# Kernel tuning notes

Measured on AMD Instinct MI355X. Metric: run time of the kernel, lower is better.

The kernel has to match this reference:

```python
import jax, jax.numpy as jnp
import numpy as np

T, B, I, H = 512, 64, 512, 1024

def setup_inputs() -> dict:
    key = jax.random.key(0)
    k1, k2, k3 = jax.random.split(key, 3)
    scale = 1.0 / np.sqrt(I + H)  # torch Linear default-ish scale
    return {
        "inputs": jax.random.normal(k1, (T, B, I), dtype=jnp.float32),
        "W": jax.random.normal(k2, (4 * H, I + H), dtype=jnp.float32) * scale,
        "b": jax.random.normal(k3, (4 * H,), dtype=jnp.float32) * scale,
    }

def reference(inputs, W, b):
    Bsz = inputs.shape[1]
    Hd = W.shape[0] // 4
    hx0 = jnp.zeros((Bsz, Hd), dtype=inputs.dtype)
    cx0 = jnp.zeros((Bsz, Hd), dtype=inputs.dtype)
    Wt = W.T  # [I+H, 4H]

    def step(carry, x):
        hx, cx = carry
        combined = jnp.concatenate([x, hx], axis=1)       # [B, I+H]
        gates = combined @ Wt + b                          # [B, 4H]
        f, i, g, o = jnp.split(gates, 4, axis=1)
        f = jax.nn.sigmoid(f)
        i = jax.nn.sigmoid(i)
        g = jnp.tanh(g)
        o = jax.nn.sigmoid(o)
        cx = f * cx + i * g
        hx = o * jnp.tanh(cx)
        return (hx, cx), hx

    (hx, cx), stacked = jax.lax.scan(step, (hx0, cx0), inputs)
    return stacked, (hx, cx)
```

## Files before the change

### kernel.cpp

```cpp
#include <hip/hip_runtime.h>
#include <stdint.h>

typedef unsigned int u32;
typedef unsigned long long u64;
typedef unsigned short u16;
typedef __attribute__((ext_vector_type(8))) short bf16x8;
typedef __attribute__((ext_vector_type(4))) float f32x4;
typedef __attribute__((ext_vector_type(2))) float f32x2;
typedef __attribute__((ext_vector_type(4))) u16 u16x4;

#define T_STEPS 512
#define BATCH   64
#define IDIM    512
#define HDIM    1024
#define GDIM    4096
#define KDIM    1536
#define NWG     256

#define GB_OFF  0u
#define XB_OFF  268435456u
#define WX_OFF  301989888u
#define HSEQ_OFF WX_OFF
#define FLG_OFF  (WX_OFF + 262144u)

__device__ __forceinline__ u16 f2bf(float f) {
  union { float f; u32 u; } v; v.f = f;
  return (u16)((v.u + 0x7fffu + ((v.u >> 16) & 1u)) >> 16);
}
__device__ __forceinline__ float bf2f(u16 h) {
  union { u32 u; float f; } v; v.u = ((u32)h) << 16; return v.f;
}

#define GLDS(g, l) __builtin_amdgcn_global_load_lds( \
    (const __attribute__((address_space(1))) u32*)(g), \
    (__attribute__((address_space(3))) u32*)(l), 16, 0, 0)

__global__ void k_cvt4(const float* __restrict__ src, u16* __restrict__ dst, int n4) {
  int i = blockIdx.x * blockDim.x + threadIdx.x;
  int stride = gridDim.x * blockDim.x;
  for (; i < n4; i += stride) {
    float4 v = reinterpret_cast<const float4*>(src)[i];
    u16x4 o; o.x = f2bf(v.x); o.y = f2bf(v.y); o.z = f2bf(v.z); o.w = f2bf(v.w);
    reinterpret_cast<u16x4*>(dst)[i] = o;
  }
}

__global__ void k_cvt_wx(const float* __restrict__ W, u16* __restrict__ wxb) {
  int i = blockIdx.x * blockDim.x + threadIdx.x;
  if (i >= GDIM * (IDIM / 4)) return;
  int row = i >> 7, cg = i & 127;
  float4 v = *reinterpret_cast<const float4*>(W + (size_t)row * KDIM + cg * 4);
  u16x4 o; o.x = f2bf(v.x); o.y = f2bf(v.y); o.z = f2bf(v.z); o.w = f2bf(v.w);
  *reinterpret_cast<u16x4*>(wxb + (size_t)row * IDIM + cg * 4) = o;
}

__global__ void k_zero(u32* __restrict__ p, int n) {
  int i = blockIdx.x * blockDim.x + threadIdx.x;
  int stride = gridDim.x * blockDim.x;
  for (; i < n; i += stride) p[i] = 0u;
}

__global__ void k_gemm_gx(const u16* __restrict__ Xb, const u16* __restrict__ Wxb,
                          const float* __restrict__ bias, u16* __restrict__ Gb) {
  __shared__ u16 lA[128 * 64];
  __shared__ u16 lB[128 * 64];
  const int tid = threadIdx.x;
  const int wv = tid >> 6, l = tid & 63;
  const int ln = l & 15, lg = l >> 4;
  const int m0 = blockIdx.x * 128, n0 = blockIdx.y * 128;
  const int wr = wv >> 1, wc = wv & 1;

  f32x4 acc[4][4];
  #pragma unroll
  for (int mi = 0; mi < 4; ++mi)
    #pragma unroll
    for (int nj = 0; nj < 4; ++nj) acc[mi][nj] = (f32x4){0.f, 0.f, 0.f, 0.f};

  for (int kt = 0; kt < 8; ++kt) {
    #pragma unroll
    for (int it = 0; it < 4; ++it) {
      int off = it * 4096 + tid * 16;
      int row = off >> 7;
      int col = (off & 127) >> 1;
      GLDS(Xb  + (size_t)(m0 + row) * IDIM + kt * 64 + col, (char*)lA + off);
      GLDS(Wxb + (size_t)(n0 + row) * IDIM + kt * 64 + col, (char*)lB + off);
    }
    asm volatile("s_waitcnt vmcnt(0)" ::: "memory");
    __syncthreads();
    #pragma unroll
    for (int ks = 0; ks < 2; ++ks) {
      bf16x8 af[4], bfr[4];
      #pragma unroll
      for (int mi = 0; mi < 4; ++mi)
        af[mi] = *reinterpret_cast<const bf16x8*>(&lA[(wr * 64 + mi * 16 + ln) * 64 + ks * 32 + lg * 8]);
      #pragma unroll
      for (int nj = 0; nj < 4; ++nj)
        bfr[nj] = *reinterpret_cast<const bf16x8*>(&lB[(wc * 64 + nj * 16 + ln) * 64 + ks * 32 + lg * 8]);
      #pragma unroll
      for (int mi = 0; mi < 4; ++mi)
        #pragma unroll
        for (int nj = 0; nj < 4; ++nj)
          acc[mi][nj] = __builtin_amdgcn_mfma_f32_16x16x32_bf16(af[mi], bfr[nj], acc[mi][nj], 0, 0, 0);
    }
    __syncthreads();
  }
  float bv[4];
  #pragma unroll
  for (int nj = 0; nj < 4; ++nj) bv[nj] = bias[n0 + wc * 64 + nj * 16 + ln];
  #pragma unroll
  for (int mi = 0; mi < 4; ++mi)
    #pragma unroll
    for (int r = 0; r < 4; ++r) {
      int m = m0 + wr * 64 + mi * 16 + lg * 4 + r;
      #pragma unroll
      for (int nj = 0; nj < 4; ++nj)
        Gb[(size_t)m * GDIM + n0 + wc * 64 + nj * 16 + ln] = f2bf(acc[mi][nj][r] + bv[nj]);
    }
}

__launch_bounds__(256, 1)
__global__ void k_lstm(const u16* __restrict__ Gb,
                       const float* __restrict__ W,
                       u16* __restrict__ hseq,
                       u32* __restrict__ flg,
                       float* __restrict__ out) {
  __shared__ f32x4 As[2048];
  const int tid = threadIdx.x;
  const int w = blockIdx.x;
  const int g = w & 7;
  const int j = w >> 3;
  const int wv = tid >> 6, l = tid & 63;
  const int n = l & 15, lg = l >> 4;
  const int h0w = j * 32 + wv * 8;
  const int jcol0 = (n >> 3) * HDIM + h0w + (n & 7);
  const int jcol1 = (2 + (n >> 3)) * HDIM + h0w + (n & 7);

  bf16x8 w0[32], w1[32];
  #pragma unroll
  for (int ks = 0; ks < 32; ++ks) {
    const float* wp = W + (size_t)jcol0 * KDIM + IDIM + ks * 32 + lg * 8;
    float4 v0 = *reinterpret_cast<const float4*>(wp);
    float4 v1 = *reinterpret_cast<const float4*>(wp + 4);
    bf16x8 fr;
    fr[0] = (short)f2bf(v0.x); fr[1] = (short)f2bf(v0.y);
    fr[2] = (short)f2bf(v0.z); fr[3] = (short)f2bf(v0.w);
    fr[4] = (short)f2bf(v1.x); fr[5] = (short)f2bf(v1.y);
    fr[6] = (short)f2bf(v1.z); fr[7] = (short)f2bf(v1.w);
    w0[ks] = fr;
  }
  #pragma unroll
  for (int ks = 0; ks < 32; ++ks) {
    const float* wp = W + (size_t)jcol1 * KDIM + IDIM + ks * 32 + lg * 8;
    float4 v0 = *reinterpret_cast<const float4*>(wp);
    float4 v1 = *reinterpret_cast<const float4*>(wp + 4);
    bf16x8 fr;
    fr[0] = (short)f2bf(v0.x); fr[1] = (short)f2bf(v0.y);
    fr[2] = (short)f2bf(v0.z); fr[3] = (short)f2bf(v0.w);
    fr[4] = (short)f2bf(v1.x); fr[5] = (short)f2bf(v1.y);
    fr[6] = (short)f2bf(v1.z); fr[7] = (short)f2bf(v1.w);
    w1[ks] = fr;
  }

  #pragma unroll
  for (int i = 0; i < 8; ++i)
    As[i * 256 + tid] = (f32x4){0.f, 0.f, 0.f, 0.f};
  __syncthreads();

  float cx[4] = {0.f, 0.f, 0.f, 0.f};

  u16 ga[4] = {0, 0, 0, 0}, gb_[4] = {0, 0, 0, 0};
  if (lg < 2) {
    #pragma unroll
    for (int r = 0; r < 4; ++r) {
      int ba = g * 8 + lg * 4 + r;
      ga[r]  = Gb[(size_t)ba * GDIM + jcol0];
      gb_[r] = Gb[(size_t)ba * GDIM + jcol1];
    }
  }

  #pragma unroll 1
  for (int t = 0; t < T_STEPS; ++t) {
    if (t > 0) {
      const u32* fp = flg + g * 32 + (l & 31);
      u32 spin = 0;
      while (true) {
        u32 v = __hip_atomic_load(fp, __ATOMIC_RELAXED, __HIP_MEMORY_SCOPE_AGENT);
        if (__all((int)(v >= (u32)t))) break;
        if (++spin > (1u << 17)) break;
      }
    }

    const char* bbase = (const char*)(hseq + (size_t)(t & 1) * (BATCH * HDIM)
                                      + (size_t)g * 8 * HDIM);
    f32x4 ld[4];
    #pragma unroll
    for (int q = 0; q < 4; ++q)
      asm volatile("global_load_dwordx4 %0, %1, off sc0 sc1"
                   : "=&v"(ld[q]) : "v"(bbase + q * 4096 + tid * 16) : "memory");
    asm volatile("s_waitcnt vmcnt(0)" ::: "memory");
    __builtin_amdgcn_sched_barrier(0);
    #pragma unroll
    for (int q = 0; q < 4; ++q) {
      int c = q * 256 + tid;
      int r = c >> 7, c8 = c & 127;
      u32 wb = (u32)(((c8 * 16 + r) << 4) ^ ((c8 & 7) << 4));
      *reinterpret_cast<f32x4*>((char*)As + wb) = ld[q];
    }
    __syncthreads();

    f32x4 c00 = {bf2f(ga[0]),  bf2f(ga[1]),  bf2f(ga[2]),  bf2f(ga[3])};
    f32x4 c10 = {bf2f(gb_[0]), bf2f(gb_[1]), bf2f(gb_[2]), bf2f(gb_[3])};
    f32x4 c01 = {0.f, 0.f, 0.f, 0.f}, c11 = c01;

    #pragma unroll
    for (int ks = 0; ks < 32; ks += 2) {
      int c8a = 4 * (ks + 0) + lg;
      int c8b = 4 * (ks + 1) + lg;
      u32 ba_ = (u32)(((c8a * 16 + n) << 4) ^ ((c8a & 7) << 4));
      u32 bb_ = (u32)(((c8b * 16 + n) << 4) ^ ((c8b & 7) << 4));
      bf16x8 f0 = *reinterpret_cast<const bf16x8*>((const char*)As + ba_);
      bf16x8 f1 = *reinterpret_cast<const bf16x8*>((const char*)As + bb_);
      c00 = __builtin_amdgcn_mfma_f32_16x16x32_bf16(f0, w0[ks + 0], c00, 0, 0, 0);
      c10 = __builtin_amdgcn_mfma_f32_16x16x32_bf16(f0, w1[ks + 0], c10, 0, 0, 0);
      c01 = __builtin_amdgcn_mfma_f32_16x16x32_bf16(f1, w0[ks + 1], c01, 0, 0, 0);
      c11 = __builtin_amdgcn_mfma_f32_16x16x32_bf16(f1, w1[ks + 1], c11, 0, 0, 0);
    }
    f32x4 t0 = c00 + c01, t1 = c10 + c11;

    u16* hw = hseq + (size_t)((t + 1) & 1) * (BATCH * HDIM);
    float o0[4], o1[4];
    #pragma unroll
    for (int r = 0; r < 4; ++r) {
      float x0 = t0[r], x1 = t1[r];
      float y0 = 1.f / (1.f + __expf(-x0));
      float s1 = (n < 8) ? 2.f * x1 : x1;
      float sg1 = 1.f / (1.f + __expf(-s1));
      float y1 = (n < 8) ? (2.f * sg1 - 1.f) : sg1;
      float iv = __shfl(y0, l | 8, 64);
      float ov = __shfl(y1, l | 8, 64);
      float c = y0 * cx[r] + iv * y1;
      cx[r] = c;
      float th = 2.f / (1.f + __expf(-2.f * c)) - 1.f;
      float hv = ov * th;

      float s0 = __shfl(hv, (l & 48) | (2 * n),     64);
      float s1v = __shfl(hv, (l & 48) | (2 * n + 1), 64);
      o0[r] = s0; o1[r] = s1v;

      if (n < 4 && lg < 2) {
        int ba = g * 8 + lg * 4 + r;
        u32 hd = (u32)f2bf(s0) | ((u32)f2bf(s1v) << 16);
        u16* dp = hw + (size_t)ba * HDIM + h0w + 2 * n;
        asm volatile("global_atomic_swap %0, %1, off"
                     :: "v"(dp), "v"(hd) : "memory");
      }
      if (t == T_STEPS - 1) {
        float q0 = __shfl(c, (l & 48) | (2 * n),     64);
        float q1 = __shfl(c, (l & 48) | (2 * n + 1), 64);
        if (n < 4 && lg < 2) {
          int ba = g * 8 + lg * 4 + r;
          float* cp = out + (size_t)T_STEPS * BATCH * HDIM + (size_t)BATCH * HDIM
                    + (size_t)ba * HDIM + h0w + 2 * n;
          f32x2 c2 = {q0, q1};
          *reinterpret_cast<f32x2*>(cp) = c2;
          float* hp = out + (size_t)T_STEPS * BATCH * HDIM
                    + (size_t)ba * HDIM + h0w + 2 * n;
          f32x2 h2 = {s0, s1v};
          *reinterpret_cast<f32x2*>(hp) = h2;
        }
      }
    }

    asm volatile("s_waitcnt vmcnt(0)" ::: "memory");
    __builtin_amdgcn_sched_barrier(0);
    __syncthreads();
    if (tid == 0) {
      u32 fv = (u32)(t + 1);
      u32* fp = flg + g * 32 + j;
      asm volatile("global_atomic_swap %0, %1, off"
                   :: "v"(fp), "v"(fv) : "memory");
    }

    if (n < 4 && lg < 2) {
      int ba0 = g * 8 + lg * 4;
      #pragma unroll
      for (int r = 0; r < 4; ++r) {
        float* op = out + ((size_t)t * BATCH + ba0 + r) * HDIM + h0w + 2 * n;
        f32x2 o2 = {o0[r], o1[r]};
        *reinterpret_cast<f32x2*>(op) = o2;
      }
    }
    {
      int tn = (t < T_STEPS - 1) ? t + 1 : t;
      if (lg < 2) {
        #pragma unroll
        for (int r = 0; r < 4; ++r) {
          int ba = g * 8 + lg * 4 + r;
          const u16* gp = Gb + ((size_t)tn * BATCH + ba) * GDIM;
          ga[r]  = gp[jcol0];
          gb_[r] = gp[jcol1];
        }
      }
    }
  }
}

extern "C" void kernel_launch(void* const* d_in, const int* in_sizes, int n_in,
                              void* d_out, int out_size, void* d_ws, size_t ws_size,
                              hipStream_t stream) {
  const float* x  = (const float*)d_in[0];
  const float* W  = (const float*)d_in[1];
  const float* b  = (const float*)d_in[2];
  float* out = (float*)d_out;
  char* ws = (char*)d_ws;

  u16* Gb   = (u16*)(ws + GB_OFF);
  u16* Xb   = (u16*)(ws + XB_OFF);
  u16* Wxb  = (u16*)(ws + WX_OFF);
  u16* hseq = (u16*)(ws + HSEQ_OFF);
  u32* flg  = (u32*)(ws + FLG_OFF);

  k_cvt4<<<2048, 256, 0, stream>>>(x, Xb, (T_STEPS * BATCH * IDIM) / 4);
  k_cvt_wx<<<(GDIM * (IDIM / 4) + 255) / 256, 256, 0, stream>>>(W, Wxb);

  dim3 gB(256, 32);
  k_gemm_gx<<<gB, 256, 0, stream>>>(Xb, Wxb, b, Gb);

  k_zero<<<64, 256, 0, stream>>>((u32*)(ws + HSEQ_OFF),
                                 (2 * BATCH * HDIM * 2 + 1024) / 4);

  k_lstm<<<NWG, 256, 0, stream>>>(Gb, (const float*)W, hseq, flg, out);
}
```

Before: 2.346 ms.

## Replace flag-based step barrier with step-tagged hidden state words

Drops the separate per-workgroup flag array and the end-of-step drain, barrier and flag store. Each hidden value is now stored as a 32-bit word whose high 16 bits carry the step number. Consumers poll the hidden-state buffer directly and re-load only the chunks whose tags are stale, then pack the bf16 halves into LDS. LDS is double-buffered by step parity so the next step's writes do not race with readers of the current buffer. The cost is twice the bytes per hidden-state exchange plus extra unpacking work, in exchange for removing one global round trip and a workgroup barrier per timestep.

```diff
diff --git a/kernel.cpp b/kernel.cpp
--- a/kernel.cpp
+++ b/kernel.cpp
@@ -21,7 +21,6 @@
 #define XB_OFF  268435456u
 #define WX_OFF  301989888u
 #define HSEQ_OFF WX_OFF
-#define FLG_OFF  (WX_OFF + 262144u)
 
 __device__ __forceinline__ u16 f2bf(float f) {
   union { float f; u32 u; } v; v.f = f;
@@ -29,6 +28,12 @@
 }
 __device__ __forceinline__ float bf2f(u16 h) {
   union { u32 u; float f; } v; v.u = ((u32)h) << 16; return v.f;
+}
+__device__ __forceinline__ u32 FU(float f) {
+  union { float f; u32 u; } v; v.f = f; return v.u;
+}
+__device__ __forceinline__ float UF(u32 u) {
+  union { u32 u; float f; } v; v.u = u; return v.f;
 }
 
 #define GLDS(g, l) __builtin_amdgcn_global_load_lds( \
@@ -121,10 +126,9 @@
 __launch_bounds__(256, 1)
 __global__ void k_lstm(const u16* __restrict__ Gb,
                        const float* __restrict__ W,
-                       u16* __restrict__ hseq,
-                       u32* __restrict__ flg,
+                       u32* __restrict__ hseq,
                        float* __restrict__ out) {
-  __shared__ f32x4 As[2048];
+  __shared__ f32x4 As[2][2048];
   const int tid = threadIdx.x;
   const int w = blockIdx.x;
   const int g = w & 7;
@@ -161,9 +165,12 @@
     w1[ks] = fr;
   }
 
-  #pragma unroll
-  for (int i = 0; i < 8; ++i)
-    As[i * 256 + tid] = (f32x4){0.f, 0.f, 0.f, 0.f};
+  {
+    f32x4* ap = &As[0][0];
+    #pragma unroll
+    for (int i = 0; i < 16; ++i)
+      ap[i * 256 + tid] = (f32x4){0.f, 0.f, 0.f, 0.f};
+  }
   __syncthreads();
 
   float cx[4] = {0.f, 0.f, 0.f, 0.f};
@@ -180,31 +187,41 @@
 
   #pragma unroll 1
   for (int t = 0; t < T_STEPS; ++t) {
-    if (t > 0) {
-      const u32* fp = flg + g * 32 + (l & 31);
-      u32 spin = 0;
-      while (true) {
-        u32 v = __hip_atomic_load(fp, __ATOMIC_RELAXED, __HIP_MEMORY_SCOPE_AGENT);
-        if (__all((int)(v >= (u32)t))) break;
-        if (++spin > (1u << 17)) break;
-      }
-    }
-
-    const char* bbase = (const char*)(hseq + (size_t)(t & 1) * (BATCH * HDIM)
-                                      + (size_t)g * 8 * HDIM);
-    f32x4 ld[4];
-    #pragma unroll
-    for (int q = 0; q < 4; ++q)
-      asm volatile("global_load_dwordx4 %0, %1, off sc0 sc1"
-                   : "=&v"(ld[q]) : "v"(bbase + q * 4096 + tid * 16) : "memory");
-    asm volatile("s_waitcnt vmcnt(0)" ::: "memory");
-    __builtin_amdgcn_sched_barrier(0);
-    #pragma unroll
-    for (int q = 0; q < 4; ++q) {
-      int c = q * 256 + tid;
-      int r = c >> 7, c8 = c & 127;
-      u32 wb = (u32)(((c8 * 16 + r) << 4) ^ ((c8 & 7) << 4));
-      *reinterpret_cast<f32x4*>((char*)As + wb) = ld[q];
+    const char* bbase = (const char*)(hseq + (size_t)(t & 1) * 65536
+                                      + (size_t)g * 8192);
+    const u32 tt = (u32)t << 16;
+    f32x4 ld[8];
+    u32 need = 0xffu, spin = 0;
+    while (true) {
+      #pragma unroll
+      for (int q = 0; q < 8; ++q)
+        if (need & (1u << q))
+          asm volatile("global_load_dwordx4 %0, %1, off sc0 sc1"
+                       : "=&v"(ld[q]) : "v"(bbase + q * 4096 + tid * 16) : "memory");
+      asm volatile("s_waitcnt vmcnt(0)" ::: "memory");
+      __builtin_amdgcn_sched_barrier(0);
+      u32 bad = 0;
+      #pragma unroll
+      for (int q = 0; q < 8; ++q)
+        if (need & (1u << q)) {
+          u32 m = ((FU(ld[q].x) ^ tt) | (FU(ld[q].y) ^ tt)
+                 | (FU(ld[q].z) ^ tt) | (FU(ld[q].w) ^ tt)) & 0xffff0000u;
+          if (m) bad |= (1u << q);
+        }
+      need = bad;
+      if (__all((int)(need == 0u))) break;
+      if (++spin > (1u << 17)) break;
+    }
+
+    char* lbase = (char*)&As[t & 1][0];
+    const int col8 = tid >> 1, half = tid & 1;
+    const u32 sbase = (u32)(col8 * 256 + half * 8);
+    #pragma unroll
+    for (int q = 0; q < 8; ++q) {
+      u32 a = FU(ld[q].x), b = FU(ld[q].y), c = FU(ld[q].z), d = FU(ld[q].w);
+      f32x2 pk2 = { UF((a & 0xffffu) | (b << 16)), UF((c & 0xffffu) | (d << 16)) };
+      u32 off = sbase + (u32)((q ^ (col8 & 7)) * 16);
+      *reinterpret_cast<f32x2*>(lbase + off) = pk2;
     }
     __syncthreads();
 
@@ -218,8 +235,8 @@
       int c8b = 4 * (ks + 1) + lg;
       u32 ba_ = (u32)(((c8a * 16 + n) << 4) ^ ((c8a & 7) << 4));
       u32 bb_ = (u32)(((c8b * 16 + n) << 4) ^ ((c8b & 7) << 4));
-      bf16x8 f0 = *reinterpret_cast<const bf16x8*>((const char*)As + ba_);
-      bf16x8 f1 = *reinterpret_cast<const bf16x8*>((const char*)As + bb_);
+      bf16x8 f0 = *reinterpret_cast<const bf16x8*>(lbase + ba_);
+      bf16x8 f1 = *reinterpret_cast<const bf16x8*>(lbase + bb_);
       c00 = __builtin_amdgcn_mfma_f32_16x16x32_bf16(f0, w0[ks + 0], c00, 0, 0, 0);
       c10 = __builtin_amdgcn_mfma_f32_16x16x32_bf16(f0, w1[ks + 0], c10, 0, 0, 0);
       c01 = __builtin_amdgcn_mfma_f32_16x16x32_bf16(f1, w0[ks + 1], c01, 0, 0, 0);
@@ -227,7 +244,8 @@
     }
     f32x4 t0 = c00 + c01, t1 = c10 + c11;
 
-    u16* hw = hseq + (size_t)((t + 1) & 1) * (BATCH * HDIM);
+    const u32 tg = ((u32)(t + 1)) << 16;
+    u32* hw = hseq + (size_t)((t + 1) & 1) * 65536 + (size_t)g * 8192;
     float o0[4], o1[4];
     #pragma unroll
     for (int r = 0; r < 4; ++r) {
@@ -248,11 +266,12 @@
       o0[r] = s0; o1[r] = s1v;
 
       if (n < 4 && lg < 2) {
-        int ba = g * 8 + lg * 4 + r;
-        u32 hd = (u32)f2bf(s0) | ((u32)f2bf(s1v) << 16);
-        u16* dp = hw + (size_t)ba * HDIM + h0w + 2 * n;
-        asm volatile("global_atomic_swap %0, %1, off"
-                     :: "v"(dp), "v"(hd) : "memory");
+        int row = lg * 4 + r;
+        u64 pk = (u64)(tg | (u32)f2bf(s0))
+               | ((u64)(tg | (u32)f2bf(s1v)) << 32);
+        u32* dp = hw + row * 1024 + h0w + 2 * n;
+        asm volatile("global_atomic_swap_x2 %0, %1, off"
+                     :: "v"(dp), "v"(pk) : "memory");
       }
       if (t == T_STEPS - 1) {
         float q0 = __shfl(c, (l & 48) | (2 * n),     64);
@@ -271,16 +290,6 @@
       }
     }
 
-    asm volatile("s_waitcnt vmcnt(0)" ::: "memory");
-    __builtin_amdgcn_sched_barrier(0);
-    __syncthreads();
-    if (tid == 0) {
-      u32 fv = (u32)(t + 1);
-      u32* fp = flg + g * 32 + j;
-      asm volatile("global_atomic_swap %0, %1, off"
-                   :: "v"(fp), "v"(fv) : "memory");
-    }
-
     if (n < 4 && lg < 2) {
       int ba0 = g * 8 + lg * 4;
       #pragma unroll
@@ -317,8 +326,7 @@
   u16* Gb   = (u16*)(ws + GB_OFF);
   u16* Xb   = (u16*)(ws + XB_OFF);
   u16* Wxb  = (u16*)(ws + WX_OFF);
-  u16* hseq = (u16*)(ws + HSEQ_OFF);
-  u32* flg  = (u32*)(ws + FLG_OFF);
+  u32* hseq = (u32*)(ws + HSEQ_OFF);
 
   k_cvt4<<<2048, 256, 0, stream>>>(x, Xb, (T_STEPS * BATCH * IDIM) / 4);
   k_cvt_wx<<<(GDIM * (IDIM / 4) + 255) / 256, 256, 0, stream>>>(W, Wxb);
@@ -326,8 +334,7 @@
   dim3 gB(256, 32);
   k_gemm_gx<<<gB, 256, 0, stream>>>(Xb, Wxb, b, Gb);
 
-  k_zero<<<64, 256, 0, stream>>>((u32*)(ws + HSEQ_OFF),
-                                 (2 * BATCH * HDIM * 2 + 1024) / 4);
-
-  k_lstm<<<NWG, 256, 0, stream>>>(Gb, (const float*)W, hseq, flg, out);
-}
+  k_zero<<<128, 256, 0, stream>>>(hseq, 2 * 8 * 8 * 1024);
+
+  k_lstm<<<NWG, 256, 0, stream>>>(Gb, (const float*)W, hseq, out);
+}
```

New measurement: 2.238 ms (median of 2 runs). 1.05x faster.
